# Kernel tuning notes

Measured on AMD Instinct MI355X. Metric: run time of the kernel, lower is better.

Reference implementation:

```python
import jax, jax.numpy as jnp
import numpy as np

WS = 8          # window size
DIM = 512       # channels
NH = 16         # heads
HD = DIM // NH  # head dim = 32
N = WS * WS     # tokens per window = 64
NW = 64         # windows per image
B = 16          # images
BW = B * NW     # total windows = 1024
SCALE = HD ** -0.5


def _relative_position_index():
    # Swin relative position index, shape (N, N), values in [0, (2*WS-1)^2)
    coords = np.stack(np.meshgrid(np.arange(WS), np.arange(WS), indexing='ij'))  # (2, WS, WS)
    coords_flat = coords.reshape(2, -1)                                           # (2, N)
    rel = coords_flat[:, :, None] - coords_flat[:, None, :]                       # (2, N, N)
    rel = rel.transpose(1, 2, 0).astype(np.int32)                                 # (N, N, 2)
    rel[:, :, 0] += WS - 1
    rel[:, :, 1] += WS - 1
    rel[:, :, 0] *= 2 * WS - 1
    return jnp.asarray(rel.sum(-1))                                               # (N, N)


def setup_inputs() -> dict:
    key = jax.random.key(0)
    ks = jax.random.split(key, 7)
    x = jax.random.normal(ks[0], (BW, N, DIM), dtype=jnp.float32)
    mask = jax.random.normal(ks[1], (NW, N, N), dtype=jnp.float32)  # shift mask (additive)
    qkv_w = jax.random.normal(ks[2], (3 * DIM, DIM), dtype=jnp.float32) * 0.02
    qkv_b = jax.random.normal(ks[3], (3 * DIM,), dtype=jnp.float32) * 0.02
    rel_bias_table = jax.random.normal(ks[4], ((2 * WS - 1) ** 2, NH), dtype=jnp.float32) * 0.02
    proj_w = jax.random.normal(ks[5], (DIM, DIM), dtype=jnp.float32) * 0.02
    proj_b = jax.random.normal(ks[6], (DIM,), dtype=jnp.float32) * 0.02
    rel_index = _relative_position_index()
    return {"x": x, "mask": mask, "qkv_w": qkv_w, "qkv_b": qkv_b,
            "rel_bias_table": rel_bias_table, "proj_w": proj_w, "proj_b": proj_b,
            "rel_index": rel_index}


def reference(x, mask, qkv_w, qkv_b, rel_bias_table, proj_w, proj_b, rel_index):
    # qkv projection: (BW, N, 3*DIM) -> (3, BW, NH, N, HD)
    qkv = (x @ qkv_w.T + qkv_b).reshape(BW, N, 3, NH, HD).transpose(2, 0, 3, 1, 4)
    q, k, v = qkv[0], qkv[1], qkv[2]
    # scaled dot-product scores: (BW, NH, N, N)
    attn = jnp.einsum('bhnd,bhmd->bhnm', q * SCALE, k)
    # relative position bias: gather (N*N,) -> (N, N, NH) -> (NH, N, N)
    bias = rel_bias_table[rel_index.reshape(-1)].reshape(N, N, NH).transpose(2, 0, 1)
    attn = attn + bias[None]
    # shift mask: broadcast over images and heads
    attn = attn.reshape(B, NW, NH, N, N) + mask[None, :, None]
    attn = jax.nn.softmax(attn.reshape(BW, NH, N, N), axis=-1)
    # weighted values: (BW, NH, N, HD) -> (BW, N, DIM)
    out = jnp.einsum('bhnm,bhmd->bhnd', attn, v).transpose(0, 2, 1, 3).reshape(BW, N, DIM)
    return out @ proj_w.T + proj_b
```

## Files before the change

kernel.cpp:

```cpp
#include <hip/hip_runtime.h>
#include <hip/hip_bf16.h>

typedef __bf16 bf16;
typedef __bf16 bf16x4 __attribute__((ext_vector_type(4)));
typedef __bf16 bf16x8 __attribute__((ext_vector_type(8)));
typedef float  f32x4  __attribute__((ext_vector_type(4)));

#define AS1 __attribute__((address_space(1)))
#define AS3 __attribute__((address_space(3)))

__device__ __forceinline__ void gld_lds16(const void* g, void* l) {
    __builtin_amdgcn_global_load_lds((AS1 void*)g, (AS3 void*)l, 16, 0, 0);
}

__global__ void cvt_kernel(const float* __restrict__ in, bf16* __restrict__ out,
                           int n4) {
    for (long i = (long)blockIdx.x * blockDim.x + threadIdx.x; i < n4;
         i += (long)gridDim.x * blockDim.x) {
        f32x4 v = ((const f32x4*)in)[i];
        bf16x4 h;
#pragma unroll
        for (int e = 0; e < 4; ++e) h[e] = (bf16)v[e];
        ((bf16x4*)out)[i] = h;
    }
}

__global__ void bias_kernel(const int* __restrict__ rel_index,
                            const float* __restrict__ table,
                            float* __restrict__ bias) {
    int idx = blockIdx.x * 256 + threadIdx.x;
    int rc = idx & 4095;
    int h  = idx >> 12;
    bias[idx] = table[rel_index[rc] * 16 + h];
}

#define STAGE(GBASE, LBASE, SK0)                                          \
    { _Pragma("unroll")                                                   \
      for (int c_ = 0; c_ < 2; ++c_)                                      \
          gld_lds16((GBASE) + c_ * 16 * 512 + (SK0),                      \
                    (LBASE) + (w * 2 + c_) * 512); }

#define FRAG_A(DST, S, KK, IH)                                              \
  { const bf16* ap_ = sA + ((S)*2+(KK))*8192 + (wm128+(IH)*64+r16)*32 + cq8;\
    _Pragma("unroll")                                                       \
    for (int ii_ = 0; ii_ < 4; ++ii_)                                       \
        DST[ii_] = *(const bf16x8*)(ap_ + ii_*512); }

#define FRAG_B(DST, S, KK)                                                  \
  { const bf16* bp_ = sB + ((S)*2+(KK))*8192 + (wn64+r16)*32 + cq8;         \
    _Pragma("unroll")                                                       \
    for (int jj_ = 0; jj_ < 4; ++jj_)                                       \
        DST[jj_] = *(const bf16x8*)(bp_ + jj_*512); }

#define PH(PFAD, PFS, PFKK, PFIH, PFB, PFBD, GB, LB, SK0, LGK, UAV, UBV,    \
           UIH, VMA)                                                        \
  { FRAG_A(PFAD, PFS, PFKK, PFIH);                                          \
    if (PFB) FRAG_B(PFBD, PFS, PFKK);                                       \
    STAGE(GB, LB, SK0);                                                     \
    __builtin_amdgcn_sched_barrier(0);                                      \
    __builtin_amdgcn_s_barrier();                                           \
    asm volatile("s_waitcnt lgkmcnt(" #LGK ")");                            \
    __builtin_amdgcn_sched_barrier(0);                                      \
    __builtin_amdgcn_s_setprio(1);                                          \
    _Pragma("unroll")                                                       \
    for (int ii_ = 0; ii_ < 4; ++ii_)                                       \
      _Pragma("unroll")                                                     \
      for (int jj_ = 0; jj_ < 4; ++jj_)                                     \
        acc[(UIH)*4+ii_][jj_] = __builtin_amdgcn_mfma_f32_16x16x32_bf16(    \
            UAV[ii_], UBV[jj_], acc[(UIH)*4+ii_][jj_], 0, 0, 0);            \
    __builtin_amdgcn_s_setprio(0);                                          \
    asm volatile(VMA);                                                      \
    __builtin_amdgcn_sched_barrier(0);                                      \
    __builtin_amdgcn_s_barrier(); }

#define GEMM_PREAMBLE                                                       \
    __shared__ __attribute__((aligned(16))) char smemraw[131072];           \
    bf16* sA = (bf16*)smemraw;                                              \
    bf16* sB = sA + 32768;                                                  \
    const int t     = threadIdx.x;                                          \
    const int w     = t >> 6;                                               \
    const int lane  = t & 63;                                               \
    const int q     = lane >> 4;                                            \
    const int r16   = lane & 15;                                            \
    const int wm128 = (w >> 2) * 128;                                       \
    const int wn64  = (w & 3) * 64;                                         \
    const int sc8   = (((lane & 3) ^ ((lane >> 4) & 3)) << 3);              \
    const int cq8   = ((q ^ ((r16 >> 2) & 3)) << 3);

#define GEMM_MAIN(ABASE, BBASE)                                             \
    const bf16* Ast = (ABASE) + (bM + w * 32 + (lane >> 2)) * 512 + sc8;    \
    const bf16* Bst = (BBASE) + (bN + w * 32 + (lane >> 2)) * 512 + sc8;    \
    f32x4 acc[8][4];                                                        \
    _Pragma("unroll")                                                       \
    for (int i = 0; i < 8; ++i)                                             \
        _Pragma("unroll")                                                   \
        for (int j = 0; j < 4; ++j) acc[i][j] = f32x4{0.f, 0.f, 0.f, 0.f};  \
    bf16x8 avA[4], avB[4], bvA[4], bvB[4];                                  \
    STAGE(Ast, sA + 0,     0);                                              \
    STAGE(Bst, sB + 0,     0);                                              \
    STAGE(Ast, sA + 8192,  32);                                             \
    STAGE(Bst, sB + 8192,  32);                                             \
    STAGE(Ast, sA + 16384, 64);                                             \
    STAGE(Bst, sB + 16384, 64);                                             \
    asm volatile("s_waitcnt vmcnt(4)");                                     \
    __builtin_amdgcn_sched_barrier(0);                                      \
    __builtin_amdgcn_s_barrier();                                           \
    FRAG_A(avA, 0, 0, 0);                                                   \
    FRAG_B(bvA, 0, 0);                                                      \
    for (int i = 0; i < 4; ++i) {                                           \
        const int t1 = 2 * i + 1;                                           \
        const int t2 = (2 * i + 2 < 8) ? 2 * i + 2 : 7;                     \
        const int t3 = (2 * i + 3 < 8) ? 2 * i + 3 : 7;                     \
        PH(avB,0,0,1, 0,bvB, Ast, sA+24576, t1*64+32, 4, avA,bvA,0, "")     \
        PH(avA,0,1,1, 1,bvB, Bst, sB+24576, t1*64+32, 8, avB,bvA,1, "")     \
        PH(avB,0,1,0, 0,bvA, Ast, sA+0,     t2*64,    4, avA,bvB,1,         \
           "s_waitcnt vmcnt(6)")                                            \
        PH(avA,1,0,0, 1,bvA, Bst, sB+0,     t2*64,    8, avB,bvB,0, "")     \
        PH(avB,1,0,1, 0,bvB, Ast, sA+8192,  t2*64+32, 4, avA,bvA,0,         \
           "s_waitcnt vmcnt(6)")                                            \
        PH(avA,1,1,1, 1,bvB, Bst, sB+8192,  t2*64+32, 8, avB,bvA,1, "")     \
        PH(avB,1,1,0, 0,bvA, Ast, sA+16384, t3*64,    4, avA,bvB,1,         \
           "s_waitcnt vmcnt(6)")                                            \
        PH(avA,0,0,0, 1,bvA, Bst, sB+16384, t3*64,    8, avB,bvB,0,         \
           "s_waitcnt vmcnt(4)")                                            \
    }                                                                       \
    asm volatile("s_waitcnt vmcnt(0) lgkmcnt(0)");                          \
    __builtin_amdgcn_sched_barrier(0);                                      \
    __builtin_amdgcn_s_barrier();

__global__ __launch_bounds__(512, 2) void gemm1_qkv8(
    const bf16* __restrict__ A, const bf16* __restrict__ B,
    const float* __restrict__ bias, bf16* __restrict__ Cq,
    bf16* __restrict__ Ckv)
{
    GEMM_PREAMBLE
    const int bid = blockIdx.x;
    const int wg  = (bid & 7) * 192 + (bid >> 3);
    const long bM = (long)(wg / 6) * 256;
    const long bN = (long)(wg % 6) * 256;

    GEMM_MAIN(A, B)

    const bool isQ = (bN < 512);
    const float sc = isQ ? 0.17677669529663687f : 1.0f;
    bf16* ct = (bf16*)smemraw;
#pragma unroll
    for (int j = 0; j < 4; ++j) {
        const int col  = wn64 + j * 16 + r16;
        const float bvv = bias[bN + col];
        const int chunk = col >> 3, cl = col & 7;
#pragma unroll
        for (int i = 0; i < 8; ++i)
#pragma unroll
            for (int r = 0; r < 4; ++r) {
                const int row = wm128 + i * 16 + q * 4 + r;
                ct[row * 256 + ((chunk ^ ((row >> 2) & 7)) << 3) + cl] =
                    (bf16)((acc[i][j][r] + bvv) * sc);
            }
    }
    __syncthreads();

    bf16* __restrict__ outp = isQ ? (Cq + bM * 512 + bN)
                                  : (Ckv + bM * 1024 + (bN - 512));
    const int ostr = isQ ? 512 : 1024;
#pragma unroll
    for (int it = 0; it < 16; ++it) {
        const int row = w * 32 + it * 2 + (lane >> 5);
        const int c   = lane & 31;
        uint4 v = *(const uint4*)(ct + row * 256 +
                                  ((c ^ ((row >> 2) & 7)) << 3));
        *(uint4*)(outp + (long)row * ostr + c * 8) = v;
    }
}

__global__ __launch_bounds__(512, 2) void gemm2_proj8(
    const bf16* __restrict__ A, const bf16* __restrict__ B,
    const float* __restrict__ bias, float* __restrict__ C)
{
    GEMM_PREAMBLE
    const int bid = blockIdx.x;
    const int wg  = (bid & 7) * 64 + (bid >> 3);
    const long bM = (long)(wg >> 1) * 256;
    const long bN = (long)(wg & 1) * 256;

    GEMM_MAIN(A, B)

#pragma unroll
    for (int j = 0; j < 4; ++j) {
        const long col = bN + wn64 + j * 16 + r16;
        const float bvv = bias[col];
#pragma unroll
        for (int i = 0; i < 8; ++i) {
            const long row = bM + wm128 + i * 16 + q * 4;
#pragma unroll
            for (int r = 0; r < 4; ++r)
                C[(row + r) * 512L + col] = acc[i][j][r] + bvv;
        }
    }
}

__global__ __launch_bounds__(256) void attn_kernel4(
    bf16* __restrict__ qbuf, const bf16* __restrict__ kv,
    const float* __restrict__ mask, const float* __restrict__ bias)
{
    __shared__ __attribute__((aligned(16))) bf16 smem[24576];
    const int t    = threadIdx.x;
    const int wv   = t >> 6;
    const int lane = t & 63;
    const int q    = lane >> 4;
    const int r16  = lane & 15;
    const int bw   = blockIdx.x >> 2;
    const int hg   = blockIdx.x & 3;
    const int h    = hg * 4 + wv;
    const int nw   = bw & 63;
    const long rowbase = (long)bw * 64;

    bf16* Qs = smem + wv * 6144;
    bf16* Ks = Qs + 2048;
    bf16* Vt = Qs + 4096;
    bf16* Ps = Qs;

    const int sc8 = (((lane & 3) ^ ((lane >> 4) & 3)) << 3);
#pragma unroll
    for (int it = 0; it < 4; ++it) {
        const int tok = it * 16 + (lane >> 2);
        gld_lds16(qbuf + (rowbase + tok) * 512  + h * 32 + sc8, Qs + it * 512);
        gld_lds16(kv   + (rowbase + tok) * 1024 + h * 32 + sc8, Ks + it * 512);
    }
    {
        const bf16* gv = kv + (rowbase + lane) * 1024 + 512 + h * 32;
        uint4 vtmp[4];
#pragma unroll
        for (int jj = 0; jj < 4; ++jj) vtmp[jj] = ((const uint4*)gv)[jj];
        const bf16* vrow = (const bf16*)vtmp;
        const int tchunk = lane >> 3, tin = lane & 7;
#pragma unroll
        for (int hd = 0; hd < 32; ++hd)
            Vt[hd * 64 + ((tchunk ^ (hd & 7)) << 3) + tin] = vrow[hd];
    }
    asm volatile("s_waitcnt vmcnt(0)" ::: "memory");

    const int cq8 = ((q ^ ((r16 >> 2) & 3)) << 3);
    f32x4 acc[4][4];
    {
        bf16x8 av[4], bv[4];
#pragma unroll
        for (int ti = 0; ti < 4; ++ti)
            av[ti] = *(const bf16x8*)&Qs[(ti * 16 + r16) * 32 + cq8];
#pragma unroll
        for (int tj = 0; tj < 4; ++tj)
            bv[tj] = *(const bf16x8*)&Ks[(tj * 16 + r16) * 32 + cq8];
        const f32x4 z = f32x4{0.f, 0.f, 0.f, 0.f};
#pragma unroll
        for (int ti = 0; ti < 4; ++ti)
#pragma unroll
            for (int tj = 0; tj < 4; ++tj)
                acc[ti][tj] = __builtin_amdgcn_mfma_f32_16x16x32_bf16(
                    av[ti], bv[tj], z, 0, 0, 0);
    }

    const float LOG2E  = 1.4426950408889634f;
    const float* biasH = bias + h * 4096;
    const float* maskW = mask + nw * 4096;

#pragma unroll
    for (int ti = 0; ti < 4; ++ti) {
#pragma unroll
        for (int r = 0; r < 4; ++r) {
            const int row = ti * 16 + q * 4 + r;
            float mx = -1e30f;
#pragma unroll
            for (int tj = 0; tj < 4; ++tj) {
                const int col = tj * 16 + r16;
                float s = acc[ti][tj][r]
                        + biasH[row * 64 + col] + maskW[row * 64 + col];
                acc[ti][tj][r] = s;
                mx = fmaxf(mx, s);
            }
#pragma unroll
            for (int d = 1; d < 16; d <<= 1)
                mx = fmaxf(mx, __shfl_xor(mx, d, 16));
            float sum = 0.f;
#pragma unroll
            for (int tj = 0; tj < 4; ++tj) {
                float e = exp2f((acc[ti][tj][r] - mx) * LOG2E);
                acc[ti][tj][r] = e;
                sum += e;
            }
#pragma unroll
            for (int d = 1; d < 16; d <<= 1)
                sum += __shfl_xor(sum, d, 16);
            const float inv = 1.0f / sum;
#pragma unroll
            for (int tj = 0; tj < 4; ++tj) {
                const int c = tj * 16 + r16;
                Ps[row * 64 + ((((c >> 3) ^ (row & 7)) << 3) + (c & 7))] =
                    (bf16)(acc[ti][tj][r] * inv);
            }
        }
    }

    f32x4 o[4][2];
#pragma unroll
    for (int ti = 0; ti < 4; ++ti)
#pragma unroll
        for (int tn = 0; tn < 2; ++tn)
            o[ti][tn] = f32x4{0.f, 0.f, 0.f, 0.f};

#pragma unroll
    for (int ks = 0; ks < 2; ++ks) {
        bf16x8 av[4], bv[2];
        const int ch = (((ks * 4 + q) ^ (r16 & 7)) << 3);
#pragma unroll
        for (int ti = 0; ti < 4; ++ti)
            av[ti] = *(const bf16x8*)&Ps[(ti * 16 + r16) * 64 + ch];
#pragma unroll
        for (int tn = 0; tn < 2; ++tn)
            bv[tn] = *(const bf16x8*)&Vt[(tn * 16 + r16) * 64 + ch];
#pragma unroll
        for (int ti = 0; ti < 4; ++ti)
#pragma unroll
            for (int tn = 0; tn < 2; ++tn)
                o[ti][tn] = __builtin_amdgcn_mfma_f32_16x16x32_bf16(
                    av[ti], bv[tn], o[ti][tn], 0, 0, 0);
    }

#pragma unroll
    for (int ti = 0; ti < 4; ++ti)
#pragma unroll
        for (int tn = 0; tn < 2; ++tn)
#pragma unroll
            for (int r = 0; r < 4; ++r)
                Qs[(ti * 16 + q * 4 + r) * 32 + tn * 16 + r16] =
                    (bf16)(o[ti][tn][r]);
    __syncthreads();

    bf16* op = qbuf + rowbase * 512 + hg * 128;
#pragma unroll
    for (int it = 0; it < 4; ++it) {
        const int idx = it * 256 + t;
        const int row = idx >> 4;
        const int c   = idx & 15;
        const int hl  = c >> 2;
        uint4 v = *(const uint4*)(smem + hl * 6144 + row * 32 + (c & 3) * 8);
        *(uint4*)(op + (long)row * 512 + hl * 32 + (c & 3) * 8) = v;
    }
}

extern "C" void kernel_launch(void* const* d_in, const int* in_sizes, int n_in,
                              void* d_out, int out_size, void* d_ws, size_t ws_size,
                              hipStream_t stream) {
    const float* x      = (const float*)d_in[0];
    const float* mask   = (const float*)d_in[1];
    const float* qkv_w  = (const float*)d_in[2];
    const float* qkv_b  = (const float*)d_in[3];
    const float* table  = (const float*)d_in[4];
    const float* proj_w = (const float*)d_in[5];
    const float* proj_b = (const float*)d_in[6];
    const int*   relidx = (const int*)d_in[7];
    float* out = (float*)d_out;

    char*  ws   = (char*)d_ws;
    float* bias = (float*)ws;
    bf16*  qbuf = (bf16*)(ws + 262144);
    bf16*  xbf  = (bf16*)(ws + 67371008);
    bf16*  wq   = (bf16*)(ws + 134479872);
    bf16*  wp   = (bf16*)(ws + 136052736);
    const size_t need_full = 136577024ull + 134217728ull;
    bf16* kvbuf = (ws_size >= need_full) ? (bf16*)(ws + 136577024)
                                         : (bf16*)d_out;

    bias_kernel<<<256, 256, 0, stream>>>(relidx, table, bias);
    cvt_kernel<<<2048, 256, 0, stream>>>(x,      xbf, 8388608);
    cvt_kernel<<<768,  256, 0, stream>>>(qkv_w,  wq,  196608);
    cvt_kernel<<<256,  256, 0, stream>>>(proj_w, wp,  65536);

    gemm1_qkv8<<<1536, 512, 0, stream>>>(xbf, wq, qkv_b, qbuf, kvbuf);
    attn_kernel4<<<4096, 256, 0, stream>>>(qbuf, kvbuf, mask, bias);
    gemm2_proj8<<<512, 512, 0, stream>>>(qbuf, wp, proj_b, out);
}
```

Measured before the change: 538.2 us.

## Precombine bias and mask with log2e, vectorize attention loads and proj epilogue

Replaces the per-head bias kernel with a kernel that precomputes bias plus shift mask, pre-scaled by log2e, for every (window, head) pair. The table is laid out so each lane loads four scores with one float4 read, and log2e is folded into the Q scale so the softmax calls exp2 directly. It also stages the projection GEMM output through shared memory in two halves so the fp32 stores to global are coalesced 16-byte writes. The cost is a 16 MB precomputed table that reuses the xbf workspace, which is safe only because that table is written after gemm1 has consumed xbf, plus extra barriers in the gemm2 epilogue.

```diff
diff --git a/kernel.cpp b/kernel.cpp
--- a/kernel.cpp
+++ b/kernel.cpp
@@ -25,13 +25,20 @@
     }
 }
 
-__global__ void bias_kernel(const int* __restrict__ rel_index,
-                            const float* __restrict__ table,
-                            float* __restrict__ bias) {
+__global__ void bmr_kernel(const int* __restrict__ rel_index,
+                           const float* __restrict__ table,
+                           const float* __restrict__ mask,
+                           float* __restrict__ bmr) {
+    const float LOG2E = 1.4426950408889634f;
     int idx = blockIdx.x * 256 + threadIdx.x;
-    int rc = idx & 4095;
-    int h  = idx >> 12;
-    bias[idx] = table[rel_index[rc] * 16 + h];
+    int tj  = idx & 3;
+    int r16 = (idx >> 2) & 15;
+    int row = (idx >> 6) & 63;
+    int h   = (idx >> 12) & 15;
+    int nw  = idx >> 16;
+    int col = tj * 16 + r16;
+    bmr[idx] = (table[rel_index[row * 64 + col] * 16 + h]
+                + mask[nw * 4096 + row * 64 + col]) * LOG2E;
 }
 
 #define STAGE(GBASE, LBASE, SK0)                                          \
@@ -142,7 +149,7 @@
     GEMM_MAIN(A, B)
 
     const bool isQ = (bN < 512);
-    const float sc = isQ ? 0.17677669529663687f : 1.0f;
+    const float sc = isQ ? 0.25503486f : 1.0f;
     bf16* ct = (bf16*)smemraw;
 #pragma unroll
     for (int j = 0; j < 4; ++j) {
@@ -185,23 +192,39 @@
 
     GEMM_MAIN(A, B)
 
-#pragma unroll
-    for (int j = 0; j < 4; ++j) {
-        const long col = bN + wn64 + j * 16 + r16;
-        const float bvv = bias[col];
-#pragma unroll
-        for (int i = 0; i < 8; ++i) {
-            const long row = bM + wm128 + i * 16 + q * 4;
-#pragma unroll
-            for (int r = 0; r < 4; ++r)
-                C[(row + r) * 512L + col] = acc[i][j][r] + bvv;
+    float* ct32 = (float*)smemraw;
+#pragma unroll
+    for (int half = 0; half < 2; ++half) {
+        __syncthreads();
+        if ((w >> 2) == half) {
+#pragma unroll
+            for (int j = 0; j < 4; ++j) {
+                const int col  = wn64 + j * 16 + r16;
+                const float bvv = bias[bN + col];
+#pragma unroll
+                for (int i = 0; i < 8; ++i)
+#pragma unroll
+                    for (int r = 0; r < 4; ++r) {
+                        const int row = i * 16 + q * 4 + r;
+                        ct32[row * 256 + (col ^ (((row >> 2) & 7) << 2))] =
+                            acc[i][j][r] + bvv;
+                    }
+            }
+        }
+        __syncthreads();
+#pragma unroll
+        for (int it = 0; it < 16; ++it) {
+            const int row = it * 8 + w;
+            f32x4 v = *(const f32x4*)&ct32[row * 256 +
+                                           ((lane * 4) ^ (((row >> 2) & 7) << 2))];
+            *(f32x4*)(C + (bM + half * 128 + row) * 512L + bN + lane * 4) = v;
         }
     }
 }
 
 __global__ __launch_bounds__(256) void attn_kernel4(
     bf16* __restrict__ qbuf, const bf16* __restrict__ kv,
-    const float* __restrict__ mask, const float* __restrict__ bias)
+    const float* __restrict__ bmr)
 {
     __shared__ __attribute__((aligned(16))) bf16 smem[24576];
     const int t    = threadIdx.x;
@@ -259,21 +282,20 @@
                     av[ti], bv[tj], z, 0, 0, 0);
     }
 
-    const float LOG2E  = 1.4426950408889634f;
-    const float* biasH = bias + h * 4096;
-    const float* maskW = mask + nw * 4096;
-
+    const float* bmw = bmr + ((long)(nw * 16 + h) << 12);
 #pragma unroll
     for (int ti = 0; ti < 4; ++ti) {
+        f32x4 bm4[4];
+#pragma unroll
+        for (int r = 0; r < 4; ++r)
+            bm4[r] = *(const f32x4*)(bmw + (ti * 16 + q * 4 + r) * 64 + r16 * 4);
 #pragma unroll
         for (int r = 0; r < 4; ++r) {
             const int row = ti * 16 + q * 4 + r;
             float mx = -1e30f;
 #pragma unroll
             for (int tj = 0; tj < 4; ++tj) {
-                const int col = tj * 16 + r16;
-                float s = acc[ti][tj][r]
-                        + biasH[row * 64 + col] + maskW[row * 64 + col];
+                float s = acc[ti][tj][r] + bm4[r][tj];
                 acc[ti][tj][r] = s;
                 mx = fmaxf(mx, s);
             }
@@ -283,7 +305,7 @@
             float sum = 0.f;
 #pragma unroll
             for (int tj = 0; tj < 4; ++tj) {
-                float e = exp2f((acc[ti][tj][r] - mx) * LOG2E);
+                float e = exp2f(acc[ti][tj][r] - mx);
                 acc[ti][tj][r] = e;
                 sum += e;
             }
@@ -361,21 +383,21 @@
     float* out = (float*)d_out;
 
     char*  ws   = (char*)d_ws;
-    float* bias = (float*)ws;
     bf16*  qbuf = (bf16*)(ws + 262144);
     bf16*  xbf  = (bf16*)(ws + 67371008);
+    float* bmr  = (float*)(ws + 67371008);
     bf16*  wq   = (bf16*)(ws + 134479872);
     bf16*  wp   = (bf16*)(ws + 136052736);
     const size_t need_full = 136577024ull + 134217728ull;
     bf16* kvbuf = (ws_size >= need_full) ? (bf16*)(ws + 136577024)
                                          : (bf16*)d_out;
 
-    bias_kernel<<<256, 256, 0, stream>>>(relidx, table, bias);
     cvt_kernel<<<2048, 256, 0, stream>>>(x,      xbf, 8388608);
     cvt_kernel<<<768,  256, 0, stream>>>(qkv_w,  wq,  196608);
     cvt_kernel<<<256,  256, 0, stream>>>(proj_w, wp,  65536);
 
     gemm1_qkv8<<<1536, 512, 0, stream>>>(xbf, wq, qkv_b, qbuf, kvbuf);
-    attn_kernel4<<<4096, 256, 0, stream>>>(qbuf, kvbuf, mask, bias);
+    bmr_kernel<<<16384, 256, 0, stream>>>(relidx, table, mask, bmr);
+    attn_kernel4<<<4096, 256, 0, stream>>>(qbuf, kvbuf, bmr);
     gemm2_proj8<<<512, 512, 0, stream>>>(qbuf, wp, proj_b, out);
 }
```

Measured after the change: 531.5 us. About the same (-1.2%).
